# Kernel optimization log

Measured on AMD Instinct MI355X. Metric: run time of the kernel, lower is better.

The kernel has to match this reference:

```python
import jax, jax.numpy as jnp
import numpy as np

B, F, S, P, E, H = 64, 32, 512, 96, 8, 2048
TOP_K = 2
ALPHA = 10.0
ENT_EPS = 1e-8
CV_EPS = 1e-10


def setup_inputs() -> dict:
    key = jax.random.key(0)
    ks = jax.random.split(key, 8)
    s = 0.02
    return {
        "x": jax.random.normal(ks[0], (B, F, S), dtype=jnp.float32),
        "time_embedding": jax.random.normal(ks[1], (B, F, S), dtype=jnp.float32),
        "Wg": jax.random.normal(ks[2], (S, E), dtype=jnp.float32) * s,
        "bg": jnp.zeros((E,), dtype=jnp.float32),
        "W1": jax.random.normal(ks[3], (E, S, H), dtype=jnp.float32) * s,
        "b1": jnp.zeros((E, H), dtype=jnp.float32),
        "W2": jax.random.normal(ks[4], (E, H, P), dtype=jnp.float32) * s,
        "b2": jnp.zeros((E, P), dtype=jnp.float32),
    }


def _gates(tf, Wg, bg):
    # tf: [F, B, S] -> logits [F, B, E]
    logits = jnp.einsum('fbs,se->fbe', tf, Wg) + bg
    # kthvalue(x, E - top_k + 1) = (E - top_k)-th entry (0-based) of ascending sort = k-th largest
    kth = jnp.sort(logits, axis=-1)[..., E - TOP_K]  # [F, B]
    mask = logits < kth[..., None]
    sm = jax.nn.softmax(logits, axis=-1)
    dec = jnp.where(mask, ALPHA * jnp.log(sm + 1.0), ALPHA * (jnp.exp(sm) - 1.0))
    return jax.nn.softmax(dec, axis=-1)  # [F, B, E]


def reference(x, time_embedding, Wg, bg, W1, b1, W2, b2):
    xf = jnp.transpose(x, (1, 0, 2))               # [F, B, S]
    tf = jnp.transpose(time_embedding, (1, 0, 2))  # [F, B, S]
    gates = _gates(tf, Wg, bg)                     # [F, B, E]

    # all experts on all features (eval mode: dropout = identity)
    h = jax.nn.gelu(jnp.einsum('fbs,esh->febh', xf, W1) + b1[None, :, None, :], approximate=False)
    eo = jnp.einsum('febh,ehp->febp', h, W2) + b2[None, :, None, :]  # [F, E, B, P]
    out = jnp.einsum('fbe,febp->fbp', gates, eo)   # gated weighted sum
    output = jnp.transpose(out, (1, 0, 2))         # [B, F, P]

    # selector loss: cv_squared of importance = gates.sum(batch) expanded over pred_len
    gsum = gates.sum(axis=1)                       # [F, E]
    imp = jnp.broadcast_to(gsum[..., None], (F, E, P)).reshape(F, E * P)
    cv = jnp.var(imp, axis=1, ddof=1) / (jnp.mean(imp, axis=1) ** 2 + CV_EPS)
    selector_loss = jnp.sum(cv)                    # loss_coef = 1.0

    # entropy loss: importance1 = gates.mean(batch) expanded over pred_len
    gmean = gates.mean(axis=1)                     # [F, E]
    imp1 = jnp.broadcast_to(gmean[..., None], (F, E, P))
    entropy_loss = jnp.sum((-imp1 * jnp.log(imp1 + ENT_EPS)).mean(axis=(1, 2)))

    return output, selector_loss, entropy_loss
```

## Files before the change

kernel.cpp:

```cpp
#include <hip/hip_runtime.h>
#include <math.h>

#define B_ 64
#define F_ 32
#define S_ 512
#define P_ 96
#define E_ 8
#define H_ 2048
#define M_ 2048

#define BM 128
#define BH 128
#define ZSPLIT 4
#define HPZ (H_ / ZSPLIT)
#define NHT (HPZ / BH)
#define NKC (S_ / 64)
#define HPITCH 136
#define W1SCALE 8.0f
#define TSTRIDE 8192

typedef __bf16 bf16x8 __attribute__((ext_vector_type(8)));
typedef __bf16 bf16x4 __attribute__((ext_vector_type(4)));
typedef float f32x4 __attribute__((ext_vector_type(4)));
typedef unsigned char u8;
typedef int i32x2 __attribute__((ext_vector_type(2)));
typedef int i32x4 __attribute__((ext_vector_type(4)));

#define MFMA16(a, b, c) __builtin_amdgcn_mfma_f32_16x16x32_bf16((a), (b), (c), 0, 0, 0)
#define MFMA8(a, b, c) __builtin_amdgcn_mfma_f32_16x16x32_fp8_fp8((a), (b), (c), 0, 0, 0)

__device__ __forceinline__ int pk_fp8x4(float a, float b, float c, float d) {
  int v = __builtin_amdgcn_cvt_pk_fp8_f32(a, b, 0, false);
  return __builtin_amdgcn_cvt_pk_fp8_f32(c, d, v, true);
}

__device__ __forceinline__ float fast_gelu(float x) {
  float e = __builtin_amdgcn_exp2f(-2.45546696f * x);
  return x * __builtin_amdgcn_rcpf(1.0f + e);
}

__global__ __launch_bounds__(256) void k_prep_w1(const float* __restrict__ W1,
                                                 u8* __restrict__ w1q) {
  __shared__ __align__(16) __bf16 btile[256 * 68];
  const int tid = threadIdx.x;
  const int e = blockIdx.x >> 5, hstrip = blockIdx.x & 31;
  const float* src = W1 + (size_t)e * S_ * H_ + hstrip * 64;
#pragma unroll
  for (int pass = 0; pass < 2; ++pass) {
    {
      int rb = tid >> 2;
      int hseg = (tid & 3) * 16;
#pragma unroll
      for (int it = 0; it < 4; ++it) {
        int r = it * 64 + rb;
        const float* srow = src + (size_t)(pass * 256 + r) * H_ + hseg;
#pragma unroll
        for (int k = 0; k < 4; ++k) {
          f32x4 v = *(const f32x4*)(srow + k * 4);
          bf16x4 o = {(__bf16)v[0], (__bf16)v[1], (__bf16)v[2], (__bf16)v[3]};
          *(bf16x4*)&btile[r * 68 + hseg + k * 4] = o;
        }
      }
    }
    __syncthreads();
#pragma unroll
    for (int i = 0; i < 4; ++i) {
      int c = tid + 256 * i;
      int tloc = c >> 8, rem = c & 255;
      int gloc = rem >> 3, u = rem & 7;
      int htile = hstrip * 4 + tloc;
      int g = pass * 32 + gloc;
      float v[16];
#pragma unroll
      for (int rr = 0; rr < 2; ++rr)
#pragma unroll
        for (int j = 0; j < 8; ++j)
          v[rr * 8 + j] = W1SCALE * (float)btile[(gloc * 8 + j) * 68 + tloc * 16 + 2 * u + rr];
      i32x4 o = {pk_fp8x4(v[0], v[1], v[2], v[3]),   pk_fp8x4(v[4], v[5], v[6], v[7]),
                 pk_fp8x4(v[8], v[9], v[10], v[11]), pk_fp8x4(v[12], v[13], v[14], v[15])};
      *(i32x4*)(w1q + ((size_t)(e * 128 + htile) * 64 + g) * 128 + u * 16) = o;
    }
    __syncthreads();
  }
}

__global__ __launch_bounds__(256) void k_prep_rest(const float* __restrict__ x,
                                                   const float* __restrict__ te,
                                                   const float* __restrict__ Wg,
                                                   const float* __restrict__ bg,
                                                   const float* __restrict__ W2,
                                                   u8* __restrict__ xq,
                                                   __bf16* __restrict__ w2t,
                                                   float* __restrict__ gates) {
  __shared__ float tile[64 * 49];
  const int blk = blockIdx.x;
  const int tid = threadIdx.x;

  if (blk < 512) {
    int e = blk >> 6, hi = (blk >> 1) & 31, ph = blk & 1;
    const float* src = W2 + (size_t)e * H_ * P_ + (size_t)(hi * 64) * P_ + ph * 48;
    {
      int h = tid & 63;
      int seg = tid >> 6;
#pragma unroll
      for (int k = 0; k < 3; ++k) {
        f32x4 v = *(const f32x4*)(src + (size_t)h * P_ + seg * 12 + k * 4);
#pragma unroll
        for (int u = 0; u < 4; ++u) tile[h * 49 + seg * 12 + k * 4 + u] = v[u];
      }
    }
    __syncthreads();
    if (tid < 192) {
      int p = tid >> 2;
      int hb = (tid & 3) * 16;
      __bf16* dst = w2t + (size_t)e * P_ * H_ + (size_t)(ph * 48 + p) * H_ + hi * 64 + hb;
      bf16x8 o0, o1;
#pragma unroll
      for (int k = 0; k < 8; ++k) o0[k] = (__bf16)tile[(hb + k) * 49 + p];
#pragma unroll
      for (int k = 0; k < 8; ++k) o1[k] = (__bf16)tile[(hb + 8 + k) * 49 + p];
      *(bf16x8*)dst = o0;
      *(bf16x8*)(dst + 8) = o1;
    }
    return;
  }
  if (blk < 1024) {
    int t = blk - 512;
    int mtile = t >> 2, gq = t & 3;
    int ml = tid & 15, gloc = tid >> 4;
    int g = gq * 16 + gloc;
    const float* srow = x + (size_t)(mtile * 16 + ml) * S_ + g * 8;
    f32x4 a = *(const f32x4*)srow;
    f32x4 b = *(const f32x4*)(srow + 4);
    i32x2 o = {pk_fp8x4(a[0], a[1], a[2], a[3]), pk_fp8x4(b[0], b[1], b[2], b[3])};
    *(i32x2*)(xq + ((size_t)(mtile * 64 + g)) * 128 + ml * 8) = o;
    return;
  }
  int wave = tid >> 6, lane = tid & 63;
  int m = (blk - 1024) * 4 + wave;
  const float* trow = te + (size_t)m * S_;
  float acc[E_];
#pragma unroll
  for (int e = 0; e < E_; ++e) acc[e] = 0.f;
  for (int s = lane; s < S_; s += 64) {
    float t = trow[s];
    const f32x4* wgr = (const f32x4*)(Wg + s * E_);
    f32x4 a = wgr[0], b = wgr[1];
    acc[0] += t * a[0]; acc[1] += t * a[1]; acc[2] += t * a[2]; acc[3] += t * a[3];
    acc[4] += t * b[0]; acc[5] += t * b[1]; acc[6] += t * b[2]; acc[7] += t * b[3];
  }
#pragma unroll
  for (int e = 0; e < E_; ++e) {
#pragma unroll
    for (int off = 32; off > 0; off >>= 1) acc[e] += __shfl_xor(acc[e], off, 64);
  }
  if (lane == 0) {
    float lg[E_];
    float m1 = -3.4e38f, m2 = -3.4e38f;
#pragma unroll
    for (int e = 0; e < E_; ++e) {
      float v = acc[e] + bg[e];
      lg[e] = v;
      if (v > m1) { m2 = m1; m1 = v; }
      else if (v > m2) { m2 = v; }
    }
    float den = 0.f, sm[E_];
#pragma unroll
    for (int e = 0; e < E_; ++e) { sm[e] = expf(lg[e] - m1); den += sm[e]; }
    float inv = 1.f / den;
    float dmax = -3.4e38f, dec[E_];
#pragma unroll
    for (int e = 0; e < E_; ++e) {
      float p = sm[e] * inv;
      float d = (lg[e] < m2) ? (10.f * logf(p + 1.f)) : (10.f * (expf(p) - 1.f));
      dec[e] = d;
      dmax = fmaxf(dmax, d);
    }
    float dden = 0.f;
#pragma unroll
    for (int e = 0; e < E_; ++e) { dec[e] = expf(dec[e] - dmax); dden += dec[e]; }
    float dinv = 1.f / dden;
#pragma unroll
    for (int e = 0; e < E_; ++e) gates[m * E_ + e] = dec[e] * dinv;
  }
}

__global__ __launch_bounds__(512, 4) void k_experts(
    const u8* __restrict__ xq,
    const u8* __restrict__ w1q,
    const __bf16* __restrict__ w2t,
    const float* __restrict__ b1,
    const float* __restrict__ b2,
    const float* __restrict__ gates,
    float* __restrict__ out)
{
  __shared__ __align__(16) __bf16 Hs[BM * HPITCH];

  const int tid = threadIdx.x;

  if (blockIdx.z == ZSPLIT) {
    if (blockIdx.x != 0 || blockIdx.y != 0) return;
    float* gsum = (float*)&Hs[0];
    float* cvs  = gsum + F_ * E_;
    float* ents = cvs + F_;
    if (tid < 256) {
      int f = tid >> 3, e = tid & 7;
      float s = 0.f;
      for (int b = 0; b < B_; ++b) s += gates[(size_t)(b * F_ + f) * E_ + e];
      gsum[f * E_ + e] = s;
    }
    __syncthreads();
    if (tid < F_) {
      float mean = 0.f;
#pragma unroll
      for (int k = 0; k < E_; ++k) mean += gsum[tid * E_ + k];
      mean *= (1.f / E_);
      float ss = 0.f;
#pragma unroll
      for (int k = 0; k < E_; ++k) { float d = gsum[tid * E_ + k] - mean; ss += d * d; }
      float var = (float)P_ * ss / (float)(E_ * P_ - 1);
      cvs[tid] = var / (mean * mean + 1e-10f);
      float ent = 0.f;
#pragma unroll
      for (int k = 0; k < E_; ++k) { float g = gsum[tid * E_ + k] * (1.f / B_); ent += -g * logf(g + 1e-8f); }
      ents[tid] = ent * (1.f / E_);
    }
    __syncthreads();
    if (tid == 0) {
      float a = 0.f, b = 0.f;
      for (int k = 0; k < F_; ++k) { a += cvs[k]; b += ents[k]; }
      out[(size_t)M_ * P_ + 0] = a;
      out[(size_t)M_ * P_ + 1] = b;
    }
    return;
  }

  const int wave = tid >> 6, lane = tid & 63;
  const int l15 = lane & 15, quad = lane >> 4;
  const int e = blockIdx.x;
  const int m0 = blockIdx.y * BM;
  const int hz = blockIdx.z * HPZ;

  const int hq = (wave & 3) * 32;
  const int mq = (wave >> 2) * 64;
  const int mt = wave & 3;
  const int ph = wave >> 2;

  const u8* w1b = w1q + (size_t)(e * 128 + (hz >> 4) + (hq >> 4)) * TSTRIDE + quad * 128 + l15 * 8;
  const u8* xb  = xq  + (size_t)((m0 >> 4) + (mq >> 4)) * TSTRIDE + quad * 128 + l15 * 8;
  const __bf16* w2z = w2t + (size_t)e * P_ * H_ + hz;

  const f32x4 fz = {0.f, 0.f, 0.f, 0.f};
  f32x4 acc2[2][3];
#pragma unroll
  for (int rt = 0; rt < 2; ++rt)
#pragma unroll
    for (int j = 0; j < 3; ++j) acc2[rt][j] = fz;

  for (int ht = 0; ht < NHT; ++ht) {
    const u8* w1h = w1b + (size_t)(ht * 8) * TSTRIDE;
    f32x4 acc1[2][4];
#pragma unroll
    for (int i = 0; i < 2; ++i)
#pragma unroll
      for (int j = 0; j < 4; ++j) acc1[i][j] = fz;

#pragma unroll 2
    for (int kc = 0; kc < NKC; ++kc) {
      long a[2][2], b[2][4];
#pragma unroll
      for (int kk = 0; kk < 2; ++kk) {
        int ko = (kc * 8 + kk * 4) * 128;
#pragma unroll
        for (int i = 0; i < 2; ++i)
          a[kk][i] = *(const long*)(w1h + (size_t)i * TSTRIDE + ko);
#pragma unroll
        for (int j = 0; j < 4; ++j)
          b[kk][j] = *(const long*)(xb + (size_t)j * TSTRIDE + ko);
      }
#pragma unroll
      for (int kk = 0; kk < 2; ++kk)
#pragma unroll
        for (int i = 0; i < 2; ++i)
#pragma unroll
          for (int j = 0; j < 4; ++j)
            acc1[i][j] = MFMA8(a[kk][i], b[kk][j], acc1[i][j]);
    }

    {
      const float* b1w = b1 + (size_t)e * H_ + hz + ht * BH + hq;
#pragma unroll
      for (int i = 0; i < 2; ++i) {
        f32x4 bv = *(const f32x4*)(b1w + i * 16 + quad * 4);
#pragma unroll
        for (int j = 0; j < 4; ++j) {
          bf16x4 hv;
#pragma unroll
          for (int r = 0; r < 4; ++r)
            hv[r] = (__bf16)fast_gelu(acc1[i][j][r] * (1.0f / W1SCALE) + bv[r]);
          *(bf16x4*)&Hs[(mq + j * 16 + l15) * HPITCH + hq + i * 16 + quad * 4] = hv;
        }
      }
    }
    __syncthreads();

    {
      const __bf16* w2c = w2z + ht * BH;
#pragma unroll
      for (int kk = 0; kk < 4; ++kk) {
        bf16x8 a0 = *(const bf16x8*)&Hs[(mt * 32 + l15) * HPITCH + kk * 32 + quad * 8];
        bf16x8 a1 = *(const bf16x8*)&Hs[(mt * 32 + 16 + l15) * HPITCH + kk * 32 + quad * 8];
#pragma unroll
        for (int j = 0; j < 3; ++j) {
          bf16x8 b = *(const bf16x8*)(w2c + (size_t)(ph * 48 + j * 16 + l15) * H_ + kk * 32 + quad * 8);
          acc2[0][j] = MFMA16(a0, b, acc2[0][j]);
          acc2[1][j] = MFMA16(a1, b, acc2[1][j]);
        }
      }
    }
    __syncthreads();
  }

#pragma unroll
  for (int rt = 0; rt < 2; ++rt) {
#pragma unroll
    for (int r = 0; r < 4; ++r) {
      int m = m0 + mt * 32 + rt * 16 + quad * 4 + r;
      float g = gates[m * E_ + e];
#pragma unroll
      for (int j = 0; j < 3; ++j) {
        int col = ph * 48 + j * 16 + l15;
        float v = acc2[rt][j][r];
        if (blockIdx.z == 0) v += b2[e * P_ + col];
        atomicAdd(&out[(size_t)m * P_ + col], g * v);
      }
    }
  }
}

extern "C" void kernel_launch(void* const* d_in, const int* in_sizes, int n_in,
                              void* d_out, int out_size, void* d_ws, size_t ws_size,
                              hipStream_t stream) {
  const float* x  = (const float*)d_in[0];
  const float* te = (const float*)d_in[1];
  const float* Wg = (const float*)d_in[2];
  const float* bg = (const float*)d_in[3];
  const float* W1 = (const float*)d_in[4];
  const float* b1 = (const float*)d_in[5];
  const float* W2 = (const float*)d_in[6];
  const float* b2 = (const float*)d_in[7];
  float* out = (float*)d_out;

  char* ws = (char*)d_ws;
  float* gates = (float*)ws;
  u8* xq       = (u8*)(ws + 65536);
  u8* w1q      = (u8*)(ws + 65536 + 1048576);
  __bf16* w2t  = (__bf16*)(ws + 65536 + 1048576 + 8388608);

  hipMemsetAsync(d_out, 0, (size_t)out_size * sizeof(float), stream);
  k_prep_w1<<<256, 256, 0, stream>>>(W1, w1q);
  k_prep_rest<<<1536, 256, 0, stream>>>(x, te, Wg, bg, W2, xq, w2t, gates);
  k_experts<<<dim3(E_, M_ / BM, ZSPLIT + 1), 512, 0, stream>>>(xq, w1q, w2t, b1, b2, gates, out);
}
```

Measured before the change: 194.2 us.

## Pre-pack W2 into MFMA fragment layout and double-buffer register loads

W2 is now pre-transposed into a fragment-ordered layout so that each lane's bf16x8 operand for the second GEMM is one contiguous 16-byte load. The first GEMM's K loop is fully unrolled with register double-buffering of the W1 and x fragments, and the W2 fragments are prefetched one step ahead, with the first batch issued before the barrier. The b1 bias load is hoisted ahead of the GEMM. Together these aim to hide global load latency behind MFMA work, at the cost of higher register pressure under launch_bounds(512,4), which could cause spills or reduce occupancy.

```diff
diff --git a/kernel.cpp b/kernel.cpp
--- a/kernel.cpp
+++ b/kernel.cpp
@@ -90,42 +90,41 @@
                                                    const float* __restrict__ bg,
                                                    const float* __restrict__ W2,
                                                    u8* __restrict__ xq,
-                                                   __bf16* __restrict__ w2t,
+                                                   __bf16* __restrict__ w2f,
                                                    float* __restrict__ gates) {
-  __shared__ float tile[64 * 49];
+  __shared__ float t2[64 * 97];
   const int blk = blockIdx.x;
   const int tid = threadIdx.x;
 
-  if (blk < 512) {
-    int e = blk >> 6, hi = (blk >> 1) & 31, ph = blk & 1;
-    const float* src = W2 + (size_t)e * H_ * P_ + (size_t)(hi * 64) * P_ + ph * 48;
+  if (blk < 256) {
+    int e = blk >> 5, hblk = blk & 31;
+    const float* src = W2 + (size_t)e * H_ * P_ + (size_t)(hblk * 64) * P_;
     {
-      int h = tid & 63;
-      int seg = tid >> 6;
-#pragma unroll
-      for (int k = 0; k < 3; ++k) {
-        f32x4 v = *(const f32x4*)(src + (size_t)h * P_ + seg * 12 + k * 4);
-#pragma unroll
-        for (int u = 0; u < 4; ++u) tile[h * 49 + seg * 12 + k * 4 + u] = v[u];
-      }
-    }
-    __syncthreads();
-    if (tid < 192) {
-      int p = tid >> 2;
-      int hb = (tid & 3) * 16;
-      __bf16* dst = w2t + (size_t)e * P_ * H_ + (size_t)(ph * 48 + p) * H_ + hi * 64 + hb;
-      bf16x8 o0, o1;
-#pragma unroll
-      for (int k = 0; k < 8; ++k) o0[k] = (__bf16)tile[(hb + k) * 49 + p];
-#pragma unroll
-      for (int k = 0; k < 8; ++k) o1[k] = (__bf16)tile[(hb + 8 + k) * 49 + p];
-      *(bf16x8*)dst = o0;
-      *(bf16x8*)(dst + 8) = o1;
+      int h = tid >> 2;
+      int pseg = (tid & 3) * 24;
+#pragma unroll
+      for (int k = 0; k < 6; ++k) {
+        f32x4 v = *(const f32x4*)(src + (size_t)h * P_ + pseg + k * 4);
+#pragma unroll
+        for (int u = 0; u < 4; ++u) t2[h * 97 + pseg + k * 4 + u] = v[u];
+      }
+    }
+    __syncthreads();
+#pragma unroll
+    for (int i = 0; i < 3; ++i) {
+      int c = tid + 256 * i;
+      int l15 = c & 15, r = c >> 4;
+      int ksl = r & 7, pt = r >> 3;
+      bf16x8 o;
+#pragma unroll
+      for (int d = 0; d < 8; ++d)
+        o[d] = (__bf16)t2[(ksl * 8 + d) * 97 + pt * 16 + l15];
+      *(bf16x8*)(w2f + ((size_t)((e * 6 + pt) * 256 + hblk * 8 + ksl)) * 128 + l15 * 8) = o;
     }
     return;
   }
-  if (blk < 1024) {
-    int t = blk - 512;
+  if (blk < 768) {
+    int t = blk - 256;
     int mtile = t >> 2, gq = t & 3;
     int ml = tid & 15, gloc = tid >> 4;
     int g = gq * 16 + gloc;
@@ -137,7 +136,7 @@
     return;
   }
   int wave = tid >> 6, lane = tid & 63;
-  int m = (blk - 1024) * 4 + wave;
+  int m = (blk - 768) * 4 + wave;
   const float* trow = te + (size_t)m * S_;
   float acc[E_];
 #pragma unroll
@@ -188,7 +187,7 @@
 __global__ __launch_bounds__(512, 4) void k_experts(
     const u8* __restrict__ xq,
     const u8* __restrict__ w1q,
-    const __bf16* __restrict__ w2t,
+    const __bf16* __restrict__ w2f,
     const float* __restrict__ b1,
     const float* __restrict__ b2,
     const float* __restrict__ gates,
@@ -240,6 +239,7 @@
   const int e = blockIdx.x;
   const int m0 = blockIdx.y * BM;
   const int hz = blockIdx.z * HPZ;
+  const int ksz = blockIdx.z * 64;
 
   const int hq = (wave & 3) * 32;
   const int mq = (wave >> 2) * 64;
@@ -248,7 +248,7 @@
 
   const u8* w1b = w1q + (size_t)(e * 128 + (hz >> 4) + (hq >> 4)) * TSTRIDE + quad * 128 + l15 * 8;
   const u8* xb  = xq  + (size_t)((m0 >> 4) + (mq >> 4)) * TSTRIDE + quad * 128 + l15 * 8;
-  const __bf16* w2z = w2t + (size_t)e * P_ * H_ + hz;
+  const __bf16* w2b = w2f + ((size_t)(e * 6 + ph * 3) * 256 + ksz + quad) * 128 + l15 * 8;
 
   const f32x4 fz = {0.f, 0.f, 0.f, 0.f};
   f32x4 acc2[2][3];
@@ -259,63 +259,84 @@
 
   for (int ht = 0; ht < NHT; ++ht) {
     const u8* w1h = w1b + (size_t)(ht * 8) * TSTRIDE;
-    f32x4 acc1[2][4];
-#pragma unroll
-    for (int i = 0; i < 2; ++i)
-#pragma unroll
-      for (int j = 0; j < 4; ++j) acc1[i][j] = fz;
-
-#pragma unroll 2
-    for (int kc = 0; kc < NKC; ++kc) {
-      long a[2][2], b[2][4];
-#pragma unroll
-      for (int kk = 0; kk < 2; ++kk) {
-        int ko = (kc * 8 + kk * 4) * 128;
-#pragma unroll
-        for (int i = 0; i < 2; ++i)
-          a[kk][i] = *(const long*)(w1h + (size_t)i * TSTRIDE + ko);
-#pragma unroll
-        for (int j = 0; j < 4; ++j)
-          b[kk][j] = *(const long*)(xb + (size_t)j * TSTRIDE + ko);
-      }
-#pragma unroll
-      for (int kk = 0; kk < 2; ++kk)
-#pragma unroll
-        for (int i = 0; i < 2; ++i)
-#pragma unroll
-          for (int j = 0; j < 4; ++j)
-            acc1[i][j] = MFMA8(a[kk][i], b[kk][j], acc1[i][j]);
-    }
-
+    f32x4 bv[2];
     {
       const float* b1w = b1 + (size_t)e * H_ + hz + ht * BH + hq;
-#pragma unroll
-      for (int i = 0; i < 2; ++i) {
-        f32x4 bv = *(const f32x4*)(b1w + i * 16 + quad * 4);
-#pragma unroll
-        for (int j = 0; j < 4; ++j) {
-          bf16x4 hv;
-#pragma unroll
-          for (int r = 0; r < 4; ++r)
-            hv[r] = (__bf16)fast_gelu(acc1[i][j][r] * (1.0f / W1SCALE) + bv[r]);
-          *(bf16x4*)&Hs[(mq + j * 16 + l15) * HPITCH + hq + i * 16 + quad * 4] = hv;
+      bv[0] = *(const f32x4*)(b1w + quad * 4);
+      bv[1] = *(const f32x4*)(b1w + 16 + quad * 4);
+    }
+
+    f32x4 acc1[2][4];
+#pragma unroll
+    for (int i = 0; i < 2; ++i)
+#pragma unroll
+      for (int j = 0; j < 4; ++j) acc1[i][j] = fz;
+
+    long a[2][2][2], b[2][2][4];
+#pragma unroll
+    for (int kk = 0; kk < 2; ++kk) {
+#pragma unroll
+      for (int i = 0; i < 2; ++i)
+        a[0][kk][i] = *(const long*)(w1h + (size_t)i * TSTRIDE + kk * 512);
+#pragma unroll
+      for (int j = 0; j < 4; ++j)
+        b[0][kk][j] = *(const long*)(xb + (size_t)j * TSTRIDE + kk * 512);
+    }
+#pragma unroll
+    for (int kc = 0; kc < NKC; ++kc) {
+      const int cur = kc & 1, nxt = cur ^ 1;
+      if (kc + 1 < NKC) {
+#pragma unroll
+        for (int kk = 0; kk < 2; ++kk) {
+#pragma unroll
+          for (int i = 0; i < 2; ++i)
+            a[nxt][kk][i] = *(const long*)(w1h + (size_t)i * TSTRIDE + (kc + 1) * 1024 + kk * 512);
+#pragma unroll
+          for (int j = 0; j < 4; ++j)
+            b[nxt][kk][j] = *(const long*)(xb + (size_t)j * TSTRIDE + (kc + 1) * 1024 + kk * 512);
         }
       }
-    }
-    __syncthreads();
-
-    {
-      const __bf16* w2c = w2z + ht * BH;
-#pragma unroll
-      for (int kk = 0; kk < 4; ++kk) {
-        bf16x8 a0 = *(const bf16x8*)&Hs[(mt * 32 + l15) * HPITCH + kk * 32 + quad * 8];
-        bf16x8 a1 = *(const bf16x8*)&Hs[(mt * 32 + 16 + l15) * HPITCH + kk * 32 + quad * 8];
-#pragma unroll
-        for (int j = 0; j < 3; ++j) {
-          bf16x8 b = *(const bf16x8*)(w2c + (size_t)(ph * 48 + j * 16 + l15) * H_ + kk * 32 + quad * 8);
-          acc2[0][j] = MFMA16(a0, b, acc2[0][j]);
-          acc2[1][j] = MFMA16(a1, b, acc2[1][j]);
-        }
+#pragma unroll
+      for (int kk = 0; kk < 2; ++kk)
+#pragma unroll
+        for (int i = 0; i < 2; ++i)
+#pragma unroll
+          for (int j = 0; j < 4; ++j)
+            acc1[i][j] = MFMA8(a[cur][kk][i], b[cur][kk][j], acc1[i][j]);
+    }
+
+#pragma unroll
+    for (int i = 0; i < 2; ++i) {
+#pragma unroll
+      for (int j = 0; j < 4; ++j) {
+        bf16x4 hv;
+#pragma unroll
+        for (int r = 0; r < 4; ++r)
+          hv[r] = (__bf16)fast_gelu(acc1[i][j][r] * (1.0f / W1SCALE) + bv[i][r]);
+        *(bf16x4*)&Hs[(mq + j * 16 + l15) * HPITCH + hq + i * 16 + quad * 4] = hv;
+      }
+    }
+
+    bf16x8 wb[2][3];
+#pragma unroll
+    for (int j = 0; j < 3; ++j)
+      wb[0][j] = *(const bf16x8*)(w2b + (size_t)j * 32768 + (size_t)(ht * 16) * 128);
+    __syncthreads();
+
+#pragma unroll
+    for (int kk = 0; kk < 4; ++kk) {
+      const int cur = kk & 1, nxt = cur ^ 1;
+      if (kk + 1 < 4) {
+#pragma unroll
+        for (int j = 0; j < 3; ++j)
+          wb[nxt][j] = *(const bf16x8*)(w2b + (size_t)j * 32768 + (size_t)(ht * 16 + (kk + 1) * 4) * 128);
+      }
+      bf16x8 a0 = *(const bf16x8*)&Hs[(mt * 32 + l15) * HPITCH + kk * 32 + quad * 8];
+      bf16x8 a1 = *(const bf16x8*)&Hs[(mt * 32 + 16 + l15) * HPITCH + kk * 32 + quad * 8];
+#pragma unroll
+      for (int j = 0; j < 3; ++j) {
+        acc2[0][j] = MFMA16(a0, wb[cur][j], acc2[0][j]);
+        acc2[1][j] = MFMA16(a1, wb[cur][j], acc2[1][j]);
       }
     }
     __syncthreads();
@@ -355,10 +376,10 @@
   float* gates = (float*)ws;
   u8* xq       = (u8*)(ws + 65536);
   u8* w1q      = (u8*)(ws + 65536 + 1048576);
-  __bf16* w2t  = (__bf16*)(ws + 65536 + 1048576 + 8388608);
+  __bf16* w2f  = (__bf16*)(ws + 65536 + 1048576 + 8388608);
 
   hipMemsetAsync(d_out, 0, (size_t)out_size * sizeof(float), stream);
   k_prep_w1<<<256, 256, 0, stream>>>(W1, w1q);
-  k_prep_rest<<<1536, 256, 0, stream>>>(x, te, Wg, bg, W2, xq, w2t, gates);
-  k_experts<<<dim3(E_, M_ / BM, ZSPLIT + 1), 512, 0, stream>>>(xq, w1q, w2t, b1, b2, gates, out);
-}
+  k_prep_rest<<<1280, 256, 0, stream>>>(x, te, Wg, bg, W2, xq, w2f, gates);
+  k_experts<<<dim3(E_, M_ / BM, ZSPLIT + 1), 512, 0, stream>>>(xq, w1q, w2f, b1, b2, gates, out);
+}
```

Measured after the change: 223.1 us. 1.15x slower.
